# Optimization experiments

Measured on AMD Instinct MI355X. Metric: run time of the kernel, lower is better.

## Reference

```python
import jax, jax.numpy as jnp
import numpy as np

B, S, T = 64, 128, 64
V, E, H, L = 32000, 512, 512, 2
PAD, BOS = 0, 1


def setup_inputs() -> dict:
    key = jax.random.key(0)
    ks = jax.random.split(key, 14)
    w = lambda k, shape: (jax.random.normal(k, shape, jnp.float32) * 0.05)
    src_emb = w(ks[0], (V, E)).at[PAD].set(0.0)
    tgt_emb = w(ks[1], (V, E)).at[PAD].set(0.0)
    enc_Wih = w(ks[2], (L, 4 * H, E))
    enc_Whh = w(ks[3], (L, 4 * H, H))
    enc_b = w(ks[4], (L, 4 * H))          # b_ih + b_hh fused
    dec_Wih = w(ks[5], (L, 4 * H, E))
    dec_Whh = w(ks[6], (L, 4 * H, H))
    dec_b = w(ks[7], (L, 4 * H))
    gen_W = w(ks[8], (V, H))
    gen_b = jnp.zeros((V,), jnp.float32)
    x_seqs = jax.random.randint(ks[9], (B, S), 0, V, jnp.int32)
    x_len = jnp.sort(jax.random.randint(ks[10], (B,), 1, S + 1, jnp.int32))[::-1]
    y_seqs = jax.random.randint(ks[11], (B, T), 0, V, jnp.int32)
    teacher = jax.random.randint(ks[12], (T - 1,), 0, 2, jnp.int32)
    return dict(x_seqs=x_seqs, x_len=x_len, y_seqs=y_seqs, teacher=teacher,
                src_emb=src_emb, tgt_emb=tgt_emb,
                enc_Wih=enc_Wih, enc_Whh=enc_Whh, enc_b=enc_b,
                dec_Wih=dec_Wih, dec_Whh=dec_Whh, dec_b=dec_b,
                gen_W=gen_W, gen_b=gen_b)


def lstm_cell(x, h, c, Wih, Whh, b):
    # torch gate order: i, f, g, o
    g = x @ Wih.T + h @ Whh.T + b
    i, f, gg, o = jnp.split(g, 4, axis=-1)
    c2 = jax.nn.sigmoid(f) * c + jax.nn.sigmoid(i) * jnp.tanh(gg)
    h2 = jax.nn.sigmoid(o) * jnp.tanh(c2)
    return h2, c2


def encode(x_seqs, x_len, src_emb, Wih, Whh, b):
    emb = src_emb[x_seqs]                                  # [B,S,E]
    mask = jnp.arange(S)[None, :] < x_len[:, None]         # [B,S] valid steps
    inp = emb.transpose(1, 0, 2)                           # [S,B,E]
    m_t = mask.T                                           # [S,B]
    hs, cs = [], []
    for l in range(L):
        def step(carry, xs, l=l):
            h, c = carry
            xt, m = xs
            h2, c2 = lstm_cell(xt, h, c, Wih[l], Whh[l], b[l])
            m = m[:, None]
            h2 = jnp.where(m, h2, h)   # freeze state past sequence length
            c2 = jnp.where(m, c2, c)
            return (h2, c2), h2
        z = jnp.zeros((B, H), inp.dtype)
        (hT, cT), out = jax.lax.scan(step, (z, z), (inp, m_t))
        inp = out
        hs.append(hT)
        cs.append(cT)
    return jnp.stack(hs), jnp.stack(cs)                    # each [L,B,H]


def reference(x_seqs, x_len, y_seqs, teacher, src_emb, tgt_emb,
              enc_Wih, enc_Whh, enc_b, dec_Wih, dec_Whh, dec_b, gen_W, gen_b):
    h0, c0 = encode(x_seqs, x_len, src_emb, enc_Wih, enc_Whh, enc_b)

    def step(carry, xs):
        h, c, inp = carry                                  # [L,B,H],[L,B,H],[B]
        y_t, tf = xs                                       # [B], scalar flag
        x = tgt_emb[inp]                                   # [B,E]
        new_h, new_c = [], []
        for l in range(L):
            hl, cl = lstm_cell(x, h[l], c[l], dec_Wih[l], dec_Whh[l], dec_b[l])
            new_h.append(hl); new_c.append(cl)
            x = hl
        logp = jax.nn.log_softmax(x @ gen_W.T + gen_b, axis=-1)   # [B,V]
        expct = jnp.take_along_axis(logp, y_t[:, None], axis=1)[:, 0]
        pred = jnp.argmax(logp, axis=1).astype(inp.dtype)
        nxt = jnp.where(tf > 0, y_t, pred)                 # scheduled sampling
        return (jnp.stack(new_h), jnp.stack(new_c), nxt), expct

    inp0 = jnp.full((B,), BOS, jnp.int32)
    _, outp = jax.lax.scan(step, (h0, c0, inp0), (y_seqs[:, 1:].T, teacher))
    return outp.T                                          # [B, T-1]
```

## Files before the change

### kernel.cpp

```cpp
#include <hip/hip_runtime.h>
#include <hip/hip_bf16.h>
#include <cstdint>
#include <cstddef>

namespace {

constexpr int B = 64, S = 128, T = 64, V = 32000, E = 512, H = 512;
constexpr int G4 = 2048;
constexpr int TM1 = T - 1;
constexpr int CHUNK = 32;
constexpr int BH = B * H;
constexpr int NT = 128;
constexpr int NTILES = V / NT;
constexpr float MARGIN = 0.02f;
constexpr unsigned NBLK = 256;

typedef __attribute__((ext_vector_type(8))) short short8v;
typedef __attribute__((ext_vector_type(4))) float f32x4;

struct GemmSh { float As[16][68]; float Bs[16][132]; };
struct StepSh { float gs[64][17]; };
struct GenSh  { float lds[64][NT + 4]; float pv1[64][4], pv2[64][4], psum[64][4], mrow[64];
                int pi1[64][4], pi2[64][4]; };
struct RedSh  { float sM[256], sS[256], red[256]; float cV[16], rV[16]; int cI[16]; int cN, nxt; };

__device__ __forceinline__ float sigf(float x) { return 1.0f / (1.0f + expf(-x)); }

__device__ __forceinline__ void split3(float w, __hip_bfloat16& a, __hip_bfloat16& b,
                                       __hip_bfloat16& c2) {
    a = __float2bfloat16(w);
    float r = w - __bfloat162float(a);
    b = __float2bfloat16(r);
    c2 = __float2bfloat16(r - __bfloat162float(b));
}


__device__ __forceinline__ unsigned ld_coh_u32(const unsigned* p) {
    unsigned v;
    asm volatile("global_load_dword %0, %1, off sc0 sc1\n\ts_waitcnt vmcnt(0)"
                 : "=v"(v) : "v"(p) : "memory");
    return v;
}
__device__ __forceinline__ void st_coh_u32(unsigned* p, unsigned v) {
    asm volatile("global_store_dword %0, %1, off sc0 sc1" :: "v"(p), "v"(v) : "memory");
}
__device__ __forceinline__ float ld_coh_f32(const float* p) {
    float v;
    asm volatile("global_load_dword %0, %1, off sc0 sc1\n\ts_waitcnt vmcnt(0)"
                 : "=v"(v) : "v"(p));
    return v;
}
__device__ __forceinline__ void st_coh_f32(float* p, float v) {
    asm volatile("global_store_dword %0, %1, off sc0 sc1" :: "v"(p), "v"(v));
}
__device__ __forceinline__ f32x4 ld_coh_f32x4(const float* p) {
    f32x4 v;
    asm volatile("global_load_dwordx4 %0, %1, off sc0 sc1\n\ts_waitcnt vmcnt(0)"
                 : "=v"(v) : "v"(p));
    return v;
}
__device__ __forceinline__ void st_coh_b16(__hip_bfloat16* p, __hip_bfloat16 v) {
    unsigned short us; __builtin_memcpy(&us, &v, 2);
    unsigned u = us;
    asm volatile("global_store_short %0, %1, off sc0 sc1" :: "v"(p), "v"(u));
}
__device__ __forceinline__ void st_coh_b128(__hip_bfloat16* p, short8v v) {
    asm volatile("global_store_dwordx4 %0, %1, off sc0 sc1" :: "v"(p), "v"(v));
}
__device__ __forceinline__ void fence_vm() {
    asm volatile("s_waitcnt vmcnt(0)" ::: "memory");
}

__device__ __forceinline__ void ldg12(const __hip_bfloat16* p0, const __hip_bfloat16* p1,
                                      const __hip_bfloat16* p2, short8v* q)
{
    asm volatile(
        "global_load_dwordx4 %0, %12, off sc0 sc1\n\t"
        "global_load_dwordx4 %1, %12, off offset:64 sc0 sc1\n\t"
        "global_load_dwordx4 %2, %12, off offset:128 sc0 sc1\n\t"
        "global_load_dwordx4 %3, %12, off offset:192 sc0 sc1\n\t"
        "global_load_dwordx4 %4, %13, off sc0 sc1\n\t"
        "global_load_dwordx4 %5, %13, off offset:64 sc0 sc1\n\t"
        "global_load_dwordx4 %6, %13, off offset:128 sc0 sc1\n\t"
        "global_load_dwordx4 %7, %13, off offset:192 sc0 sc1\n\t"
        "global_load_dwordx4 %8, %14, off sc0 sc1\n\t"
        "global_load_dwordx4 %9, %14, off offset:64 sc0 sc1\n\t"
        "global_load_dwordx4 %10, %14, off offset:128 sc0 sc1\n\t"
        "global_load_dwordx4 %11, %14, off offset:192 sc0 sc1\n\t"
        "s_waitcnt vmcnt(0)"
        : "=&v"(q[0]), "=&v"(q[1]), "=&v"(q[2]), "=&v"(q[3]),
          "=&v"(q[4]), "=&v"(q[5]), "=&v"(q[6]), "=&v"(q[7]),
          "=&v"(q[8]), "=&v"(q[9]), "=&v"(q[10]), "=&v"(q[11])
        : "v"(p0), "v"(p1), "v"(p2));
}

__device__ __forceinline__ void ldg16(const __hip_bfloat16* p0, const __hip_bfloat16* p1,
                                      const __hip_bfloat16* p2, const __hip_bfloat16* p3,
                                      short8v* q)
{
    asm volatile(
        "global_load_dwordx4 %0, %16, off sc0 sc1\n\t"
        "global_load_dwordx4 %1, %16, off offset:64 sc0 sc1\n\t"
        "global_load_dwordx4 %2, %16, off offset:128 sc0 sc1\n\t"
        "global_load_dwordx4 %3, %16, off offset:192 sc0 sc1\n\t"
        "global_load_dwordx4 %4, %17, off sc0 sc1\n\t"
        "global_load_dwordx4 %5, %17, off offset:64 sc0 sc1\n\t"
        "global_load_dwordx4 %6, %17, off offset:128 sc0 sc1\n\t"
        "global_load_dwordx4 %7, %17, off offset:192 sc0 sc1\n\t"
        "global_load_dwordx4 %8, %18, off sc0 sc1\n\t"
        "global_load_dwordx4 %9, %18, off offset:64 sc0 sc1\n\t"
        "global_load_dwordx4 %10, %18, off offset:128 sc0 sc1\n\t"
        "global_load_dwordx4 %11, %18, off offset:192 sc0 sc1\n\t"
        "global_load_dwordx4 %12, %19, off sc0 sc1\n\t"
        "global_load_dwordx4 %13, %19, off offset:64 sc0 sc1\n\t"
        "global_load_dwordx4 %14, %19, off offset:128 sc0 sc1\n\t"
        "global_load_dwordx4 %15, %19, off offset:192 sc0 sc1\n\t"
        "s_waitcnt vmcnt(0)"
        : "=&v"(q[0]), "=&v"(q[1]), "=&v"(q[2]), "=&v"(q[3]),
          "=&v"(q[4]), "=&v"(q[5]), "=&v"(q[6]), "=&v"(q[7]),
          "=&v"(q[8]), "=&v"(q[9]), "=&v"(q[10]), "=&v"(q[11]),
          "=&v"(q[12]), "=&v"(q[13]), "=&v"(q[14]), "=&v"(q[15])
        : "v"(p0), "v"(p1), "v"(p2), "v"(p3));
}

__device__ __forceinline__ void ldg8(const __hip_bfloat16* p0, const __hip_bfloat16* p1,
                                     short8v* q)
{
    asm volatile(
        "global_load_dwordx4 %0, %8, off sc0 sc1\n\t"
        "global_load_dwordx4 %1, %8, off offset:64 sc0 sc1\n\t"
        "global_load_dwordx4 %2, %8, off offset:128 sc0 sc1\n\t"
        "global_load_dwordx4 %3, %8, off offset:192 sc0 sc1\n\t"
        "global_load_dwordx4 %4, %9, off sc0 sc1\n\t"
        "global_load_dwordx4 %5, %9, off offset:64 sc0 sc1\n\t"
        "global_load_dwordx4 %6, %9, off offset:128 sc0 sc1\n\t"
        "global_load_dwordx4 %7, %9, off offset:192 sc0 sc1\n\t"
        "s_waitcnt vmcnt(0)"
        : "=&v"(q[0]), "=&v"(q[1]), "=&v"(q[2]), "=&v"(q[3]),
          "=&v"(q[4]), "=&v"(q[5]), "=&v"(q[6]), "=&v"(q[7])
        : "v"(p0), "v"(p1));
}

__device__ __forceinline__ void gbar(unsigned* flags, unsigned* rel, unsigned& ep)
{
    unsigned tgt = ++ep;
    fence_vm();
    __syncthreads();
    const int tid = threadIdx.x;
    if (blockIdx.x == 0) {
        if (tid > 0) {
            int spins = 0;
            while (ld_coh_u32(&flags[tid * 32]) < tgt) {
                if (spins < 8) __builtin_amdgcn_s_sleep(1);
                else           __builtin_amdgcn_s_sleep(32);
                if (++spins > (1 << 16)) break;
            }
        }
        __syncthreads();
        st_coh_u32(&rel[tid * 32], tgt);
    } else {
        if (tid == 0) {
            st_coh_u32(&flags[blockIdx.x * 32], tgt);
            int spins = 0;
            while (ld_coh_u32(&rel[blockIdx.x * 32]) < tgt) {
                if (spins < 8) __builtin_amdgcn_s_sleep(1);
                else           __builtin_amdgcn_s_sleep(32);
                if (++spins > (1 << 16)) break;
            }
        }
        __syncthreads();
    }
}

__global__ __launch_bounds__(256)
void split_dec_k(const float* __restrict__ Wih, const float* __restrict__ Whh,
                 const float* __restrict__ bsrc,
                 __hip_bfloat16* __restrict__ P0, __hip_bfloat16* __restrict__ P1,
                 __hip_bfloat16* __restrict__ P2, float* __restrict__ bint)
{
    int row = blockIdx.x;
    int l = row >> 11, jp = row & 2047;
    int kh = jp >> 2, g = jp & 3, src = g * 512 + kh;
    const float* wih = Wih + ((size_t)l * 2048 + src) * 512;
    const float* whh = Whh + ((size_t)l * 2048 + src) * 512;
    size_t ro = (size_t)row * 1024;
    for (int k = threadIdx.x; k < 1024; k += 256) {
        float w = (k < 512) ? whh[k] : wih[k - 512];
        __hip_bfloat16 a, b, c2; split3(w, a, b, c2);
        P0[ro + k] = a; P1[ro + k] = b; P2[ro + k] = c2;
    }
    if (threadIdx.x == 0) bint[row] = bsrc[l * 2048 + src];
}

__global__ __launch_bounds__(256)
void split_enc_k(const float* __restrict__ Whh,
                 __hip_bfloat16* __restrict__ P0, __hip_bfloat16* __restrict__ P1,
                 __hip_bfloat16* __restrict__ P2)
{
    int row = blockIdx.x;
    int kh = row >> 2, g = row & 3, src = g * 512 + kh;
    const float* whh = Whh + (size_t)src * 512;
    size_t ro = (size_t)row * 512;
    for (int k = threadIdx.x; k < 512; k += 256) {
        __hip_bfloat16 a, b, c2; split3(whh[k], a, b, c2);
        P0[ro + k] = a; P1[ro + k] = b; P2[ro + k] = c2;
    }
}

__device__ void gemm_tile(char* shraw, const float* __restrict__ A,
                          const float* __restrict__ Wt, const float* __restrict__ bias,
                          float* __restrict__ C,
                          const int* __restrict__ xseq, int m0, int bx, int by)
{
    GemmSh* sh = reinterpret_cast<GemmSh*>(shraw);
    constexpr int K = 512, BK = 16;
    int tid = threadIdx.x;
    int bm = by * 64, bn = bx * 128;
    int tx = tid & 15, ty = tid >> 4;
    float acc[4][8] = {};

    int lm = tid >> 2, lk = (tid & 3) << 2;
    const float* Arow;
    {
        int mg = m0 + bm + lm; int tt = mg >> 6, b = mg & 63;
        Arow = A + (size_t)xseq[b * S + tt] * K;
    }
    int ln = tid >> 1, lkb = (tid & 1) << 3;
    const float* Brow = Wt + (size_t)(bn + ln) * K;

    for (int k0 = 0; k0 < K; k0 += BK) {
        float4 av = *(const float4*)(Arow + k0 + lk);
        sh->As[lk + 0][lm] = av.x; sh->As[lk + 1][lm] = av.y;
        sh->As[lk + 2][lm] = av.z; sh->As[lk + 3][lm] = av.w;
        float4 bv0 = *(const float4*)(Brow + k0 + lkb);
        float4 bv1 = *(const float4*)(Brow + k0 + lkb + 4);
        sh->Bs[lkb + 0][ln] = bv0.x; sh->Bs[lkb + 1][ln] = bv0.y;
        sh->Bs[lkb + 2][ln] = bv0.z; sh->Bs[lkb + 3][ln] = bv0.w;
        sh->Bs[lkb + 4][ln] = bv1.x; sh->Bs[lkb + 5][ln] = bv1.y;
        sh->Bs[lkb + 6][ln] = bv1.z; sh->Bs[lkb + 7][ln] = bv1.w;
        __syncthreads();
#pragma unroll
        for (int kk = 0; kk < BK; ++kk) {
            const float4 a4  = *(const float4*)&sh->As[kk][ty * 4];
            const float4 b4a = *(const float4*)&sh->Bs[kk][tx * 8];
            const float4 b4b = *(const float4*)&sh->Bs[kk][tx * 8 + 4];
            const float a[4]  = {a4.x, a4.y, a4.z, a4.w};
            const float bb[8] = {b4a.x, b4a.y, b4a.z, b4a.w,
                                 b4b.x, b4b.y, b4b.z, b4b.w};
#pragma unroll
            for (int i = 0; i < 4; ++i)
#pragma unroll
                for (int j = 0; j < 8; ++j)
                    acc[i][j] = fmaf(a[i], bb[j], acc[i][j]);
        }
        __syncthreads();
    }
#pragma unroll
    for (int i = 0; i < 4; ++i) {
        size_t crow = (size_t)(bm + ty * 4 + i) * G4;
#pragma unroll
        for (int j = 0; j < 8; ++j) {
            int cg = bn + tx * 8 + j;
            int jp = ((cg & 511) << 2) | (cg >> 9);
            st_coh_f32(C + crow + jp, acc[i][j] + bias[cg]);
        }
    }
}

template<int KHALF, bool ADDXC, bool MASK>
__device__ void step_body(char* shraw, int blk,
    const __hip_bfloat16* __restrict__ hA0, const __hip_bfloat16* __restrict__ hA1,
    const __hip_bfloat16* __restrict__ hA2,
    const __hip_bfloat16* __restrict__ xA0, const __hip_bfloat16* __restrict__ xA1,
    const __hip_bfloat16* __restrict__ xA2,
    const __hip_bfloat16* __restrict__ W0, const __hip_bfloat16* __restrict__ W1,
    const __hip_bfloat16* __restrict__ W2,
    const float* __restrict__ addsrc, const float* __restrict__ h_in,
    float* __restrict__ h_out, float* __restrict__ c,
    __hip_bfloat16* __restrict__ o0, __hip_bfloat16* __restrict__ o1,
    __hip_bfloat16* __restrict__ o2,
    const int* __restrict__ x_len, int t)
{
    StepSh* sh = reinterpret_cast<StepSh*>(shraw);
    int tid = threadIdx.x;
    int wave = tid >> 6, lane = tid & 63;
    int lr = lane & 15, kg = (lane >> 4) * 8;
    int arow = wave * 16 + lr;
    int brow = blk * 16 + lr;
    const int KW = 512 * KHALF;

    f32x4 acc0 = {0,0,0,0}, acc1 = {0,0,0,0}, acc2 = {0,0,0,0};
    const size_t aoff = (size_t)arow * 512 + kg;
    const size_t boff = (size_t)brow * KW + kg;

#pragma unroll
    for (int g = 0; g < KHALF * 4; ++g) {
        const __hip_bfloat16 *A0, *A1, *A2; size_t go;
        if (KHALF == 2 && g >= 4) { A0 = xA0; A1 = xA1; A2 = xA2;
                                    go = aoff + (size_t)(g - 4) * 128; }
        else                      { A0 = hA0; A1 = hA1; A2 = hA2;
                                    go = aoff + (size_t)g * 128; }
        short8v q[12];
        ldg12(A0 + go, A1 + go, A2 + go, q);
#pragma unroll
        for (int j = 0; j < 4; ++j) {
            int k0 = g * 128 + j * 32;
            short8v b0 = *(const short8v*)(W0 + boff + k0);
            short8v b1 = *(const short8v*)(W1 + boff + k0);
            short8v b2 = *(const short8v*)(W2 + boff + k0);
            short8v a0 = q[j], a1 = q[4 + j], a2 = q[8 + j];
            acc0 = __builtin_amdgcn_mfma_f32_16x16x32_bf16(a0, b0, acc0, 0, 0, 0);
            acc1 = __builtin_amdgcn_mfma_f32_16x16x32_bf16(a0, b1, acc1, 0, 0, 0);
            acc2 = __builtin_amdgcn_mfma_f32_16x16x32_bf16(a1, b0, acc2, 0, 0, 0);
            acc0 = __builtin_amdgcn_mfma_f32_16x16x32_bf16(a1, b1, acc0, 0, 0, 0);
            acc1 = __builtin_amdgcn_mfma_f32_16x16x32_bf16(a0, b2, acc1, 0, 0, 0);
            acc2 = __builtin_amdgcn_mfma_f32_16x16x32_bf16(a2, b0, acc2, 0, 0, 0);
        }
    }
    int rb = (lane >> 4) * 4;
#pragma unroll
    for (int r = 0; r < 4; ++r)
        sh->gs[wave * 16 + rb + r][lr] = acc0[r] + acc1[r] + acc2[r];
    __syncthreads();

    int b = tid >> 2, khl = tid & 3;
    int khg = blk * 4 + khl;
    f32x4 add;
    if (ADDXC) add = ld_coh_f32x4(addsrc + (size_t)b * G4 + (size_t)khg * 4);
    else       add = *(const f32x4*)(addsrc + (size_t)khg * 4);
    float gi = sh->gs[b][khl * 4 + 0] + add[0];
    float gf = sh->gs[b][khl * 4 + 1] + add[1];
    float gg = sh->gs[b][khl * 4 + 2] + add[2];
    float go2 = sh->gs[b][khl * 4 + 3] + add[3];
    size_t idx = (size_t)b * H + khg;
    float cold = ld_coh_f32(c + idx);
    float c2 = sigf(gf) * cold + sigf(gi) * tanhf(gg);
    float h2 = sigf(go2) * tanhf(c2);
    if (MASK) {
        bool mk = t < x_len[b];
        if (!mk) { h2 = ld_coh_f32(h_in + idx); c2 = cold; }
    }
    if (h_out) st_coh_f32(h_out + idx, h2);
    st_coh_f32(c + idx, c2);
    __hip_bfloat16 s0, s1, s2; split3(h2, s0, s1, s2);
    st_coh_b16(o0 + idx, s0); st_coh_b16(o1 + idx, s1); st_coh_b16(o2 + idx, s2);
}

__device__ void gen_body(char* shraw, int bid,
                         const __hip_bfloat16* __restrict__ hbf,
                         const __hip_bfloat16* __restrict__ Wbf,
                         const float* __restrict__ genb,
                         float* __restrict__ part)
{
    GenSh* sh = reinterpret_cast<GenSh*>(shraw);
    int tid = threadIdx.x;
    int wave = tid >> 6, lane = tid & 63;
    int n0 = bid * NT;
    int lr = lane & 15;
    int kg = (lane >> 4) * 8;

    f32x4 acc[4][2];
    const f32x4 zero = {0.f, 0.f, 0.f, 0.f};
#pragma unroll
    for (int i = 0; i < 4; ++i)
#pragma unroll
        for (int j = 0; j < 2; ++j) acc[i][j] = zero;

    const __hip_bfloat16* Arow = hbf + (size_t)lr * 512 + kg;
    const __hip_bfloat16* Brow = Wbf + (size_t)(n0 + wave * 32 + lr) * 512 + kg;
#pragma unroll
    for (int g = 0; g < 4; ++g) {
        short8v qa[16], qb[8];
        ldg16(Arow + g * 128, Arow + 8192 + g * 128,
              Arow + 16384 + g * 128, Arow + 24576 + g * 128, qa);
        ldg8(Brow + g * 128, Brow + 8192 + g * 128, qb);
#pragma unroll
        for (int j = 0; j < 4; ++j) {
#pragma unroll
            for (int mf = 0; mf < 4; ++mf)
#pragma unroll
                for (int nf = 0; nf < 2; ++nf)
                    acc[mf][nf] = __builtin_amdgcn_mfma_f32_16x16x32_bf16(
                        qa[mf * 4 + j], qb[nf * 4 + j], acc[mf][nf], 0, 0, 0);
        }
    }
#pragma unroll
    for (int nf = 0; nf < 2; ++nf) {
        int colLocal = wave * 32 + nf * 16 + lr;
        float bias = genb[n0 + colLocal];
#pragma unroll
        for (int mf = 0; mf < 4; ++mf) {
#pragma unroll
            for (int r = 0; r < 4; ++r) {
                int row = mf * 16 + (lane >> 4) * 4 + r;
                sh->lds[row][colLocal] = acc[mf][nf][r] + bias;
            }
        }
    }
    __syncthreads();

    int row = tid >> 2, q = tid & 3;
    int cbase = q * 32;
    float v1 = -3.4e38f, v2 = -3.4e38f; int i1 = 0x7fffffff, i2 = 0x7fffffff;
    for (int c = 0; c < 32; ++c) {
        float v = sh->lds[row][cbase + c];
        int ci = cbase + c;
        if (v > v1 || (v == v1 && ci < i1)) { v2 = v1; i2 = i1; v1 = v; i1 = ci; }
        else if (v > v2 || (v == v2 && ci < i2)) { v2 = v; i2 = ci; }
    }
    sh->pv1[row][q] = v1; sh->pi1[row][q] = i1; sh->pv2[row][q] = v2; sh->pi2[row][q] = i2;
    __syncthreads();

    float t1 = -3.4e38f, t2 = -3.4e38f; int j1 = 0x7fffffff, j2 = 0x7fffffff;
    if (q == 0) {
        for (int k = 0; k < 4; ++k) {
            float a1 = sh->pv1[row][k]; int a1i = sh->pi1[row][k];
            float a2 = sh->pv2[row][k]; int a2i = sh->pi2[row][k];
            if (a1 > t1 || (a1 == t1 && a1i < j1)) { t2 = t1; j2 = j1; t1 = a1; j1 = a1i; }
            else if (a1 > t2 || (a1 == t2 && a1i < j2)) { t2 = a1; j2 = a1i; }
            if (a2 > t1 || (a2 == t1 && a2i < j1)) { t2 = t1; j2 = j1; t1 = a2; j1 = a2i; }
            else if (a2 > t2 || (a2 == t2 && a2i < j2)) { t2 = a2; j2 = a2i; }
        }
        sh->mrow[row] = t1;
    }
    __syncthreads();
    float m = sh->mrow[row];
    float s = 0.f;
    for (int c = 0; c < 32; ++c) s += expf(sh->lds[row][cbase + c] - m);
    sh->psum[row][q] = s;
    __syncthreads();
    if (q == 0) {
        float sum = sh->psum[row][0] + sh->psum[row][1] + sh->psum[row][2] + sh->psum[row][3];
        float* p = part + ((size_t)bid * B + row) * 6;
        st_coh_f32(p + 0, t1);
        st_coh_f32(p + 1, t2);
        st_coh_u32((unsigned*)(p + 2), (unsigned)(n0 + j1));
        st_coh_u32((unsigned*)(p + 3), (unsigned)(n0 + j2));
        st_coh_f32(p + 4, sum);
    }
}

__device__ void reduce_body(char* shraw, int b,
                            const float* __restrict__ part,
                            const float* __restrict__ h,
                            const float* __restrict__ genW, const float* __restrict__ genb,
                            const float* __restrict__ tgt_emb,
                            const int* __restrict__ y_seqs, const int* __restrict__ teacher,
                            float* __restrict__ outp,
                            __hip_bfloat16* __restrict__ xp0, __hip_bfloat16* __restrict__ xp1,
                            __hip_bfloat16* __restrict__ xp2, int t)
{
    RedSh* sh = reinterpret_cast<RedSh*>(shraw);
    int tid = threadIdx.x;
    int y = y_seqs[b * T + t + 1];
    const float* hrow = h + (size_t)b * 512;
    float h_a = ld_coh_f32(hrow + tid);
    float h_b = ld_coh_f32(hrow + tid + 256);

    float p_top1 = -3.4e38f, p_top2 = -3.4e38f, p_sum = 0.f;
    int p_i1 = 0x7fffffff, p_i2 = 0x7fffffff;
    if (tid < NTILES) {
        const float* p = part + ((size_t)tid * B + b) * 6;
        f32x4 v4 = ld_coh_f32x4(p);
        p_top1 = v4[0]; p_top2 = v4[1];
        p_i1 = __float_as_int(v4[2]);
        p_i2 = __float_as_int(v4[3]);
        p_sum = ld_coh_f32(p + 4);
    }
    sh->sM[tid] = p_top1; __syncthreads();
    for (int o = 128; o; o >>= 1) { if (tid < o) sh->sM[tid] = fmaxf(sh->sM[tid], sh->sM[tid + o]); __syncthreads(); }
    float M = sh->sM[0];
    if (tid == 0) sh->cN = 0;
    __syncthreads();

    float Ssum = (tid < NTILES) ? p_sum * expf(p_top1 - M) : 0.f;
    if (tid < NTILES) {
        if (p_top1 >= M - MARGIN) { int j = atomicAdd(&sh->cN, 1); if (j < 16) { sh->cV[j] = p_top1; sh->cI[j] = p_i1; } }
        if (p_top2 >= M - MARGIN) { int j = atomicAdd(&sh->cN, 1); if (j < 16) { sh->cV[j] = p_top2; sh->cI[j] = p_i2; } }
    }
    sh->sS[tid] = Ssum; __syncthreads();
    for (int o = 128; o; o >>= 1) { if (tid < o) sh->sS[tid] += sh->sS[tid + o]; __syncthreads(); }
    float lse = M + logf(sh->sS[0]);
    int nc = sh->cN < 16 ? sh->cN : 16;

    {
        const float* wrow = genW + (size_t)y * 512;
        float s = fmaf(h_a, wrow[tid], 0.f) + h_b * wrow[tid + 256];
        sh->red[tid] = s; __syncthreads();
        for (int o = 128; o; o >>= 1) { if (tid < o) sh->red[tid] += sh->red[tid + o]; __syncthreads(); }
        if (tid == 0) outp[b * TM1 + t] = sh->red[0] + genb[y] - lse;
        __syncthreads();
    }
    if (nc > 1) {
        for (int j = 0; j < nc; ++j) {
            const float* wrow = genW + (size_t)sh->cI[j] * 512;
            float s = fmaf(h_a, wrow[tid], 0.f) + h_b * wrow[tid + 256];
            sh->red[tid] = s; __syncthreads();
            for (int o = 128; o; o >>= 1) { if (tid < o) sh->red[tid] += sh->red[tid + o]; __syncthreads(); }
            if (tid == 0) sh->rV[j] = sh->red[0] + genb[sh->cI[j]];
            __syncthreads();
        }
    }
    if (tid == 0) {
        int winner;
        if (nc == 1) winner = sh->cI[0];
        else {
            float bv = -3.4e38f; int bi = 0x7fffffff;
            for (int j = 0; j < nc; ++j)
                if (sh->rV[j] > bv || (sh->rV[j] == bv && sh->cI[j] < bi)) { bv = sh->rV[j]; bi = sh->cI[j]; }
            winner = bi;
        }
        sh->nxt = (teacher[t] > 0) ? y : winner;
    }
    __syncthreads();
    int tok = sh->nxt;
    for (int k = tid; k < 512; k += 256) {
        float w = tgt_emb[(size_t)tok * 512 + k];
        __hip_bfloat16 s0, s1, s2; split3(w, s0, s1, s2);
        st_coh_b16(xp0 + (size_t)b * 512 + k, s0);
        st_coh_b16(xp1 + (size_t)b * 512 + k, s1);
        st_coh_b16(xp2 + (size_t)b * 512 + k, s2);
    }
}

struct Args {
    const int *x_seqs, *x_len, *y_seqs, *teacher;
    const float *src_emb, *tgt_emb, *eWih, *eb, *genW, *genb;
    float* Xc;
    const __hip_bfloat16 *eP0, *eP1, *eP2;
    const __hip_bfloat16 *e1P0, *e1P1, *e1P2;
    const float* ebint;
    const __hip_bfloat16 *dP0, *dP1, *dP2;
    const float* bint;
    float *hf32, *cbuf, *dech1;
    __hip_bfloat16 *P, *xP, *Wbf;
    float* part;
    float* outp;
    unsigned *flags, *rel;
};

__global__ __launch_bounds__(256, 1)
void persist_k(Args a)
{
    __shared__ __align__(16) char shpool[40960];
    unsigned ep = 0;
    const int bid = blockIdx.x;
    const int tid = threadIdx.x;
    const int gtid = bid * 256 + tid;
    const int GS = NBLK * 256;

    auto Pl = [&](int l, int slot, int pl) {
        return a.P + (((size_t)(l * 2 + slot)) * 3 + pl) * BH; };

    for (int i = gtid; i < BH; i += GS) {
        st_coh_f32(a.hf32 + i, 0.f); st_coh_f32(a.hf32 + 2 * BH + i, 0.f);
        st_coh_f32(a.cbuf + i, 0.f); st_coh_f32(a.cbuf + BH + i, 0.f);
    }
    {
        unsigned* p0 = (unsigned*)Pl(0, 0, 0);
        unsigned* p1 = (unsigned*)Pl(1, 0, 0);
        for (int i = gtid; i < 3 * BH / 2; i += GS) { st_coh_u32(p0 + i, 0u); st_coh_u32(p1 + i, 0u); }
    }
    gbar(a.flags, a.rel, ep);

    for (int c0 = 0; c0 < S; c0 += CHUNK) {
        for (int tile = bid; tile < 512; tile += NBLK)
            gemm_tile(shpool, a.src_emb, a.eWih, a.eb, a.Xc,
                      a.x_seqs, c0 * B, tile & 15, tile >> 4);
        gbar(a.flags, a.rel, ep);
        for (int tl = 0; tl < CHUNK; ++tl) {
            int t = c0 + tl;
            if (bid < 128) {
                step_body<1, true, true>(shpool, bid,
                    Pl(0, t & 1, 0), Pl(0, t & 1, 1), Pl(0, t & 1, 2),
                    nullptr, nullptr, nullptr,
                    a.eP0, a.eP1, a.eP2,
                    a.Xc + (size_t)tl * B * G4,
                    a.hf32 + (size_t)(t & 1) * BH, a.hf32 + (size_t)((t + 1) & 1) * BH,
                    a.cbuf,
                    Pl(0, (t + 1) & 1, 0), Pl(0, (t + 1) & 1, 1), Pl(0, (t + 1) & 1, 2),
                    a.x_len, t);
            } else if (t >= 1) {
                int u = t - 1;
                step_body<2, false, true>(shpool, bid - 128,
                    Pl(1, u & 1, 0), Pl(1, u & 1, 1), Pl(1, u & 1, 2),
                    Pl(0, t & 1, 0), Pl(0, t & 1, 1), Pl(0, t & 1, 2),
                    a.e1P0, a.e1P1, a.e1P2,
                    a.ebint,
                    a.hf32 + (size_t)(2 + (u & 1)) * BH, a.hf32 + (size_t)(2 + ((u + 1) & 1)) * BH,
                    a.cbuf + BH,
                    Pl(1, (u + 1) & 1, 0), Pl(1, (u + 1) & 1, 1), Pl(1, (u + 1) & 1, 2),
                    a.x_len, u);
            }
            gbar(a.flags, a.rel, ep);
        }
    }
    if (bid < 128) {
        int u = S - 1;
        step_body<2, false, true>(shpool, bid,
            Pl(1, u & 1, 0), Pl(1, u & 1, 1), Pl(1, u & 1, 2),
            Pl(0, (u + 1) & 1, 0), Pl(0, (u + 1) & 1, 1), Pl(0, (u + 1) & 1, 2),
            a.e1P0, a.e1P1, a.e1P2,
            a.ebint,
            a.hf32 + (size_t)(2 + (u & 1)) * BH, a.hf32 + (size_t)(2 + ((u + 1) & 1)) * BH,
            a.cbuf + BH,
            Pl(1, (u + 1) & 1, 0), Pl(1, (u + 1) & 1, 1), Pl(1, (u + 1) & 1, 2),
            a.x_len, u);
    }
    gbar(a.flags, a.rel, ep);

    {
        const int N8 = V * E / 8;
        for (int i = gtid; i < N8; i += GS) {
            float4 x = *(const float4*)(a.genW + (size_t)i * 8);
            float4 y = *(const float4*)(a.genW + (size_t)i * 8 + 4);
            __hip_bfloat16 tmp[8];
            tmp[0] = __float2bfloat16(x.x); tmp[1] = __float2bfloat16(x.y);
            tmp[2] = __float2bfloat16(x.z); tmp[3] = __float2bfloat16(x.w);
            tmp[4] = __float2bfloat16(y.x); tmp[5] = __float2bfloat16(y.y);
            tmp[6] = __float2bfloat16(y.z); tmp[7] = __float2bfloat16(y.w);
            st_coh_b128(a.Wbf + (size_t)i * 8, *(const short8v*)tmp);
        }
        for (int i = gtid; i < BH; i += GS) {
            int k = i & 511;
            float w = a.tgt_emb[512 + k];
            __hip_bfloat16 s0, s1, s2; split3(w, s0, s1, s2);
            st_coh_b16(a.xP + i, s0);
            st_coh_b16(a.xP + BH + i, s1);
            st_coh_b16(a.xP + 2 * BH + i, s2);
        }
    }
    gbar(a.flags, a.rel, ep);

    for (int t = 0; t < TM1; ++t) {
        int si = t & 1, so = si ^ 1;
        if (bid < 128)
            step_body<2, false, false>(shpool, bid,
                Pl(0, si, 0), Pl(0, si, 1), Pl(0, si, 2),
                a.xP, a.xP + BH, a.xP + 2 * BH,
                a.dP0, a.dP1, a.dP2, a.bint,
                nullptr, nullptr, a.cbuf,
                Pl(0, so, 0), Pl(0, so, 1), Pl(0, so, 2),
                nullptr, 0);
        gbar(a.flags, a.rel, ep);
        if (bid < 128)
            step_body<2, false, false>(shpool, bid,
                Pl(1, si, 0), Pl(1, si, 1), Pl(1, si, 2),
                Pl(0, so, 0), Pl(0, so, 1), Pl(0, so, 2),
                a.dP0 + (size_t)G4 * 1024, a.dP1 + (size_t)G4 * 1024,
                a.dP2 + (size_t)G4 * 1024, a.bint + G4,
                nullptr, a.dech1, a.cbuf + BH,
                Pl(1, so, 0), Pl(1, so, 1), Pl(1, so, 2),
                nullptr, 0);
        gbar(a.flags, a.rel, ep);
        if (bid < NTILES)
            gen_body(shpool, bid, Pl(1, so, 0), a.Wbf, a.genb, a.part);
        gbar(a.flags, a.rel, ep);
        if (bid < B)
            reduce_body(shpool, bid, a.part, a.dech1, a.genW, a.genb, a.tgt_emb,
                        a.y_seqs, a.teacher, a.outp,
                        a.xP, a.xP + BH, a.xP + 2 * BH, t);
        gbar(a.flags, a.rel, ep);
    }
}

}

extern "C" void kernel_launch(void* const* d_in, const int* in_sizes, int n_in,
                              void* d_out, int out_size, void* d_ws, size_t ws_size,
                              hipStream_t stream)
{
    (void)in_sizes; (void)n_in; (void)out_size;
    const int*   x_seqs  = (const int*)  d_in[0];
    const int*   x_len   = (const int*)  d_in[1];
    const int*   y_seqs  = (const int*)  d_in[2];
    const int*   teacher = (const int*)  d_in[3];
    const float* src_emb = (const float*)d_in[4];
    const float* tgt_emb = (const float*)d_in[5];
    const float* eWih    = (const float*)d_in[6];
    const float* eWhh    = (const float*)d_in[7];
    const float* eb      = (const float*)d_in[8];
    const float* dWih    = (const float*)d_in[9];
    const float* dWhh    = (const float*)d_in[10];
    const float* db      = (const float*)d_in[11];
    const float* genW    = (const float*)d_in[12];
    const float* genb    = (const float*)d_in[13];

    float* w = (float*)d_ws;
    size_t off = 0;
    auto take = [&](size_t n) { float* p = w + off; off += n; return p; };
    auto takeb = [&](size_t n) { return (__hip_bfloat16*)take((n + 1) / 2); };

    unsigned* flags = (unsigned*)take(256 * 32);
    unsigned* rel   = (unsigned*)take(256 * 32);
    float* Xc = take((size_t)CHUNK * B * G4);
    __hip_bfloat16* eP0  = takeb((size_t)G4 * 512);
    __hip_bfloat16* eP1  = takeb((size_t)G4 * 512);
    __hip_bfloat16* eP2  = takeb((size_t)G4 * 512);
    __hip_bfloat16* e1P0 = takeb((size_t)G4 * 1024);
    __hip_bfloat16* e1P1 = takeb((size_t)G4 * 1024);
    __hip_bfloat16* e1P2 = takeb((size_t)G4 * 1024);
    float* ebint = take((size_t)G4);
    __hip_bfloat16* dP0 = takeb((size_t)2 * G4 * 1024);
    __hip_bfloat16* dP1 = takeb((size_t)2 * G4 * 1024);
    __hip_bfloat16* dP2 = takeb((size_t)2 * G4 * 1024);
    float* bint  = take(2 * (size_t)G4);
    float* hf32  = take(4 * (size_t)BH);
    float* cbuf  = take(2 * (size_t)BH);
    float* dech1 = take((size_t)BH);
    __hip_bfloat16* P  = takeb((size_t)12 * BH);
    __hip_bfloat16* xP = takeb((size_t)3 * BH);
    float* part_f = take((size_t)NTILES * B * 6);
    if (ws_size < off * sizeof(float)) return;

    dim3 tpb256(256);
    split_enc_k<<<dim3(G4), tpb256, 0, stream>>>(eWhh, eP0, eP1, eP2);
    split_dec_k<<<dim3(G4), tpb256, 0, stream>>>(
        eWih + (size_t)G4 * E, eWhh + (size_t)G4 * E, eb + G4, e1P0, e1P1, e1P2, ebint);
    split_dec_k<<<dim3(2 * G4), tpb256, 0, stream>>>(
        dWih, dWhh, db, dP0, dP1, dP2, bint);
    hipError_t _e = hipMemsetAsync(flags, 0, 2 * 256 * 32 * sizeof(unsigned), stream);
    (void)_e;

    Args a;
    a.x_seqs = x_seqs; a.x_len = x_len; a.y_seqs = y_seqs; a.teacher = teacher;
    a.src_emb = src_emb; a.tgt_emb = tgt_emb; a.eWih = eWih; a.eb = eb;
    a.genW = genW; a.genb = genb;
    a.Xc = Xc;
    a.eP0 = eP0; a.eP1 = eP1; a.eP2 = eP2;
    a.e1P0 = e1P0; a.e1P1 = e1P1; a.e1P2 = e1P2; a.ebint = ebint;
    a.dP0 = dP0; a.dP1 = dP1; a.dP2 = dP2; a.bint = bint;
    a.hf32 = hf32; a.cbuf = cbuf; a.dech1 = dech1;
    a.P = P; a.xP = xP;
    a.Wbf = (__hip_bfloat16*)Xc;
    a.part = part_f;
    a.outp = (float*)d_out;
    a.flags = flags; a.rel = rel;

    persist_k<<<dim3(NBLK), tpb256, 0, stream>>>(a);
}
```

Baseline: 10.36 ms.

## Widen LSTM step tiles to 64 columns and version decoder state buffers per step

Each step block now computes 64 gate columns instead of 16, so the recurrent steps run on 32 blocks instead of 128, with vectorized state stores. Decoder hidden, input and embedding planes become per-timestep versioned buffers, which lets the step and reduce kernels read them through normal cached loads instead of coherent loads. The generator now reads A fragments directly instead of bulk coherent loads, and the barrier spin uses a fixed sleep. The aim is to cut coherent-load traffic and per-step sync cost, at the price of fewer active blocks and more workspace memory.

New measurement: 22.24 ms. 2.15x slower.

```diff
diff --git a/kernel.cpp b/kernel.cpp
--- a/kernel.cpp
+++ b/kernel.cpp
@@ -17,9 +17,10 @@
 
 typedef __attribute__((ext_vector_type(8))) short short8v;
 typedef __attribute__((ext_vector_type(4))) float f32x4;
+typedef __attribute__((ext_vector_type(2))) unsigned u32x2;
 
 struct GemmSh { float As[16][68]; float Bs[16][132]; };
-struct StepSh { float gs[64][17]; };
+struct StepSh { float gs[64][68]; };
 struct GenSh  { float lds[64][NT + 4]; float pv1[64][4], pv2[64][4], psum[64][4], mrow[64];
                 int pi1[64][4], pi2[64][4]; };
 struct RedSh  { float sM[256], sS[256], red[256]; float cV[16], rV[16]; int cI[16]; int cN, nxt; };
@@ -33,7 +34,9 @@
     b = __float2bfloat16(r);
     c2 = __float2bfloat16(r - __bfloat162float(b));
 }
-
+__device__ __forceinline__ unsigned short bf16bits(__hip_bfloat16 v) {
+    unsigned short u; __builtin_memcpy(&u, &v, 2); return u;
+}
 
 __device__ __forceinline__ unsigned ld_coh_u32(const unsigned* p) {
     unsigned v;
@@ -59,10 +62,11 @@
                  : "=v"(v) : "v"(p));
     return v;
 }
-__device__ __forceinline__ void st_coh_b16(__hip_bfloat16* p, __hip_bfloat16 v) {
-    unsigned short us; __builtin_memcpy(&us, &v, 2);
-    unsigned u = us;
-    asm volatile("global_store_short %0, %1, off sc0 sc1" :: "v"(p), "v"(u));
+__device__ __forceinline__ void st_coh_f32x4(float* p, f32x4 v) {
+    asm volatile("global_store_dwordx4 %0, %1, off sc0 sc1" :: "v"(p), "v"(v));
+}
+__device__ __forceinline__ void st_coh_b64(__hip_bfloat16* p, u32x2 v) {
+    asm volatile("global_store_dwordx2 %0, %1, off sc0 sc1" :: "v"(p), "v"(v));
 }
 __device__ __forceinline__ void st_coh_b128(__hip_bfloat16* p, short8v v) {
     asm volatile("global_store_dwordx4 %0, %1, off sc0 sc1" :: "v"(p), "v"(v));
@@ -94,35 +98,6 @@
         : "v"(p0), "v"(p1), "v"(p2));
 }
 
-__device__ __forceinline__ void ldg16(const __hip_bfloat16* p0, const __hip_bfloat16* p1,
-                                      const __hip_bfloat16* p2, const __hip_bfloat16* p3,
-                                      short8v* q)
-{
-    asm volatile(
-        "global_load_dwordx4 %0, %16, off sc0 sc1\n\t"
-        "global_load_dwordx4 %1, %16, off offset:64 sc0 sc1\n\t"
-        "global_load_dwordx4 %2, %16, off offset:128 sc0 sc1\n\t"
-        "global_load_dwordx4 %3, %16, off offset:192 sc0 sc1\n\t"
-        "global_load_dwordx4 %4, %17, off sc0 sc1\n\t"
-        "global_load_dwordx4 %5, %17, off offset:64 sc0 sc1\n\t"
-        "global_load_dwordx4 %6, %17, off offset:128 sc0 sc1\n\t"
-        "global_load_dwordx4 %7, %17, off offset:192 sc0 sc1\n\t"
-        "global_load_dwordx4 %8, %18, off sc0 sc1\n\t"
-        "global_load_dwordx4 %9, %18, off offset:64 sc0 sc1\n\t"
-        "global_load_dwordx4 %10, %18, off offset:128 sc0 sc1\n\t"
-        "global_load_dwordx4 %11, %18, off offset:192 sc0 sc1\n\t"
-        "global_load_dwordx4 %12, %19, off sc0 sc1\n\t"
-        "global_load_dwordx4 %13, %19, off offset:64 sc0 sc1\n\t"
-        "global_load_dwordx4 %14, %19, off offset:128 sc0 sc1\n\t"
-        "global_load_dwordx4 %15, %19, off offset:192 sc0 sc1\n\t"
-        "s_waitcnt vmcnt(0)"
-        : "=&v"(q[0]), "=&v"(q[1]), "=&v"(q[2]), "=&v"(q[3]),
-          "=&v"(q[4]), "=&v"(q[5]), "=&v"(q[6]), "=&v"(q[7]),
-          "=&v"(q[8]), "=&v"(q[9]), "=&v"(q[10]), "=&v"(q[11]),
-          "=&v"(q[12]), "=&v"(q[13]), "=&v"(q[14]), "=&v"(q[15])
-        : "v"(p0), "v"(p1), "v"(p2), "v"(p3));
-}
-
 __device__ __forceinline__ void ldg8(const __hip_bfloat16* p0, const __hip_bfloat16* p1,
                                      short8v* q)
 {
@@ -151,9 +126,8 @@
         if (tid > 0) {
             int spins = 0;
             while (ld_coh_u32(&flags[tid * 32]) < tgt) {
-                if (spins < 8) __builtin_amdgcn_s_sleep(1);
-                else           __builtin_amdgcn_s_sleep(32);
-                if (++spins > (1 << 16)) break;
+                __builtin_amdgcn_s_sleep(4);
+                if (++spins > (1 << 17)) break;
             }
         }
         __syncthreads();
@@ -163,9 +137,8 @@
             st_coh_u32(&flags[blockIdx.x * 32], tgt);
             int spins = 0;
             while (ld_coh_u32(&rel[blockIdx.x * 32]) < tgt) {
-                if (spins < 8) __builtin_amdgcn_s_sleep(1);
-                else           __builtin_amdgcn_s_sleep(32);
-                if (++spins > (1 << 16)) break;
+                __builtin_amdgcn_s_sleep(4);
+                if (++spins > (1 << 17)) break;
             }
         }
         __syncthreads();
@@ -267,7 +240,7 @@
     }
 }
 
-template<int KHALF, bool ADDXC, bool MASK>
+template<int KHALF, bool ADDXC, bool MASK, bool CACHED>
 __device__ void step_body(char* shraw, int blk,
     const __hip_bfloat16* __restrict__ hA0, const __hip_bfloat16* __restrict__ hA1,
     const __hip_bfloat16* __restrict__ hA2,
@@ -286,12 +259,19 @@
     int wave = tid >> 6, lane = tid & 63;
     int lr = lane & 15, kg = (lane >> 4) * 8;
     int arow = wave * 16 + lr;
-    int brow = blk * 16 + lr;
     const int KW = 512 * KHALF;
-
-    f32x4 acc0 = {0,0,0,0}, acc1 = {0,0,0,0}, acc2 = {0,0,0,0};
     const size_t aoff = (size_t)arow * 512 + kg;
-    const size_t boff = (size_t)brow * KW + kg;
+    size_t boff[4];
+#pragma unroll
+    for (int ct = 0; ct < 4; ++ct)
+        boff[ct] = (size_t)(blk * 64 + ct * 16 + lr) * KW + kg;
+
+    f32x4 acc[4][3];
+    const f32x4 zero = {0.f, 0.f, 0.f, 0.f};
+#pragma unroll
+    for (int ct = 0; ct < 4; ++ct)
+#pragma unroll
+        for (int p = 0; p < 3; ++p) acc[ct][p] = zero;
 
 #pragma unroll
     for (int g = 0; g < KHALF * 4; ++g) {
@@ -300,50 +280,85 @@
                                     go = aoff + (size_t)(g - 4) * 128; }
         else                      { A0 = hA0; A1 = hA1; A2 = hA2;
                                     go = aoff + (size_t)g * 128; }
-        short8v q[12];
-        ldg12(A0 + go, A1 + go, A2 + go, q);
+        short8v qa[12];
+        if (CACHED) {
+#pragma unroll
+            for (int j = 0; j < 4; ++j) {
+                qa[j]     = *(const short8v*)(A0 + go + j * 32);
+                qa[4 + j] = *(const short8v*)(A1 + go + j * 32);
+                qa[8 + j] = *(const short8v*)(A2 + go + j * 32);
+            }
+        } else {
+            ldg12(A0 + go, A1 + go, A2 + go, qa);
+        }
 #pragma unroll
         for (int j = 0; j < 4; ++j) {
             int k0 = g * 128 + j * 32;
-            short8v b0 = *(const short8v*)(W0 + boff + k0);
-            short8v b1 = *(const short8v*)(W1 + boff + k0);
-            short8v b2 = *(const short8v*)(W2 + boff + k0);
-            short8v a0 = q[j], a1 = q[4 + j], a2 = q[8 + j];
-            acc0 = __builtin_amdgcn_mfma_f32_16x16x32_bf16(a0, b0, acc0, 0, 0, 0);
-            acc1 = __builtin_amdgcn_mfma_f32_16x16x32_bf16(a0, b1, acc1, 0, 0, 0);
-            acc2 = __builtin_amdgcn_mfma_f32_16x16x32_bf16(a1, b0, acc2, 0, 0, 0);
-            acc0 = __builtin_amdgcn_mfma_f32_16x16x32_bf16(a1, b1, acc0, 0, 0, 0);
-            acc1 = __builtin_amdgcn_mfma_f32_16x16x32_bf16(a0, b2, acc1, 0, 0, 0);
-            acc2 = __builtin_amdgcn_mfma_f32_16x16x32_bf16(a2, b0, acc2, 0, 0, 0);
+            short8v a0 = qa[j], a1 = qa[4 + j], a2 = qa[8 + j];
+#pragma unroll
+            for (int ct = 0; ct < 4; ++ct) {
+                short8v b0 = *(const short8v*)(W0 + boff[ct] + k0);
+                short8v b1 = *(const short8v*)(W1 + boff[ct] + k0);
+                short8v b2 = *(const short8v*)(W2 + boff[ct] + k0);
+                acc[ct][0] = __builtin_amdgcn_mfma_f32_16x16x32_bf16(a0, b0, acc[ct][0], 0, 0, 0);
+                acc[ct][1] = __builtin_amdgcn_mfma_f32_16x16x32_bf16(a0, b1, acc[ct][1], 0, 0, 0);
+                acc[ct][2] = __builtin_amdgcn_mfma_f32_16x16x32_bf16(a1, b0, acc[ct][2], 0, 0, 0);
+                acc[ct][0] = __builtin_amdgcn_mfma_f32_16x16x32_bf16(a1, b1, acc[ct][0], 0, 0, 0);
+                acc[ct][1] = __builtin_amdgcn_mfma_f32_16x16x32_bf16(a0, b2, acc[ct][1], 0, 0, 0);
+                acc[ct][2] = __builtin_amdgcn_mfma_f32_16x16x32_bf16(a2, b0, acc[ct][2], 0, 0, 0);
+            }
         }
     }
     int rb = (lane >> 4) * 4;
 #pragma unroll
     for (int r = 0; r < 4; ++r)
-        sh->gs[wave * 16 + rb + r][lr] = acc0[r] + acc1[r] + acc2[r];
+#pragma unroll
+        for (int ct = 0; ct < 4; ++ct)
+            sh->gs[wave * 16 + rb + r][ct * 16 + lr] =
+                acc[ct][0][r] + acc[ct][1][r] + acc[ct][2][r];
     __syncthreads();
 
-    int b = tid >> 2, khl = tid & 3;
-    int khg = blk * 4 + khl;
-    f32x4 add;
-    if (ADDXC) add = ld_coh_f32x4(addsrc + (size_t)b * G4 + (size_t)khg * 4);
-    else       add = *(const f32x4*)(addsrc + (size_t)khg * 4);
-    float gi = sh->gs[b][khl * 4 + 0] + add[0];
-    float gf = sh->gs[b][khl * 4 + 1] + add[1];
-    float gg = sh->gs[b][khl * 4 + 2] + add[2];
-    float go2 = sh->gs[b][khl * 4 + 3] + add[3];
-    size_t idx = (size_t)b * H + khg;
-    float cold = ld_coh_f32(c + idx);
-    float c2 = sigf(gf) * cold + sigf(gi) * tanhf(gg);
-    float h2 = sigf(go2) * tanhf(c2);
-    if (MASK) {
-        bool mk = t < x_len[b];
-        if (!mk) { h2 = ld_coh_f32(h_in + idx); c2 = cold; }
-    }
-    if (h_out) st_coh_f32(h_out + idx, h2);
-    st_coh_f32(c + idx, c2);
-    __hip_bfloat16 s0, s1, s2; split3(h2, s0, s1, s2);
-    st_coh_b16(o0 + idx, s0); st_coh_b16(o1 + idx, s1); st_coh_b16(o2 + idx, s2);
+    int b = tid >> 2, q = tid & 3;
+    int m0 = q * 4;
+    int khg0 = blk * 16 + m0;
+    size_t idx0 = (size_t)b * H + khg0;
+    f32x4 cold4 = ld_coh_f32x4(c + idx0);
+    f32x4 hin4 = {0.f, 0.f, 0.f, 0.f};
+    bool mk = true;
+    if (MASK) { mk = (t < x_len[b]); if (!mk) hin4 = ld_coh_f32x4(h_in + idx0); }
+    f32x4 h4, c4;
+#pragma unroll
+    for (int kk = 0; kk < 4; ++kk) {
+        int m = m0 + kk;
+        f32x4 add;
+        if (ADDXC) add = ld_coh_f32x4(addsrc + (size_t)b * G4 + (size_t)(khg0 + kk) * 4);
+        else       add = *(const f32x4*)(addsrc + (size_t)(khg0 + kk) * 4);
+        float gi  = sh->gs[b][m * 4 + 0] + add[0];
+        float gf  = sh->gs[b][m * 4 + 1] + add[1];
+        float gg  = sh->gs[b][m * 4 + 2] + add[2];
+        float go2 = sh->gs[b][m * 4 + 3] + add[3];
+        float c2 = sigf(gf) * cold4[kk] + sigf(gi) * tanhf(gg);
+        float h2 = sigf(go2) * tanhf(c2);
+        if (MASK && !mk) { h2 = hin4[kk]; c2 = cold4[kk]; }
+        h4[kk] = h2; c4[kk] = c2;
+    }
+    st_coh_f32x4(c + idx0, c4);
+    if (h_out) st_coh_f32x4(h_out + idx0, h4);
+    unsigned short s0b[4], s1b[4], s2b[4];
+#pragma unroll
+    for (int kk = 0; kk < 4; ++kk) {
+        __hip_bfloat16 s0, s1, s2; split3(h4[kk], s0, s1, s2);
+        s0b[kk] = bf16bits(s0); s1b[kk] = bf16bits(s1); s2b[kk] = bf16bits(s2);
+    }
+    u32x2 p0 = {(unsigned)s0b[0] | ((unsigned)s0b[1] << 16),
+                (unsigned)s0b[2] | ((unsigned)s0b[3] << 16)};
+    u32x2 p1 = {(unsigned)s1b[0] | ((unsigned)s1b[1] << 16),
+                (unsigned)s1b[2] | ((unsigned)s1b[3] << 16)};
+    u32x2 p2 = {(unsigned)s2b[0] | ((unsigned)s2b[1] << 16),
+                (unsigned)s2b[2] | ((unsigned)s2b[3] << 16)};
+    st_coh_b64(o0 + idx0, p0);
+    st_coh_b64(o1 + idx0, p1);
+    st_coh_b64(o2 + idx0, p2);
 }
 
 __device__ void gen_body(char* shraw, int bid,
@@ -370,18 +385,18 @@
     const __hip_bfloat16* Brow = Wbf + (size_t)(n0 + wave * 32 + lr) * 512 + kg;
 #pragma unroll
     for (int g = 0; g < 4; ++g) {
-        short8v qa[16], qb[8];
-        ldg16(Arow + g * 128, Arow + 8192 + g * 128,
-              Arow + 16384 + g * 128, Arow + 24576 + g * 128, qa);
+        short8v qb[8];
         ldg8(Brow + g * 128, Brow + 8192 + g * 128, qb);
 #pragma unroll
         for (int j = 0; j < 4; ++j) {
 #pragma unroll
-            for (int mf = 0; mf < 4; ++mf)
+            for (int mf = 0; mf < 4; ++mf) {
+                short8v a = *(const short8v*)(Arow + (size_t)mf * 8192 + g * 128 + j * 32);
 #pragma unroll
                 for (int nf = 0; nf < 2; ++nf)
                     acc[mf][nf] = __builtin_amdgcn_mfma_f32_16x16x32_bf16(
-                        qa[mf * 4 + j], qb[nf * 4 + j], acc[mf][nf], 0, 0, 0);
+                        a, qb[nf * 4 + j], acc[mf][nf], 0, 0, 0);
+            }
         }
     }
 #pragma unroll
@@ -454,8 +469,8 @@
     int tid = threadIdx.x;
     int y = y_seqs[b * T + t + 1];
     const float* hrow = h + (size_t)b * 512;
-    float h_a = ld_coh_f32(hrow + tid);
-    float h_b = ld_coh_f32(hrow + tid + 256);
+    float h_a = hrow[tid];
+    float h_b = hrow[tid + 256];
 
     float p_top1 = -3.4e38f, p_top2 = -3.4e38f, p_sum = 0.f;
     int p_i1 = 0x7fffffff, p_i2 = 0x7fffffff;
@@ -517,9 +532,12 @@
     for (int k = tid; k < 512; k += 256) {
         float w = tgt_emb[(size_t)tok * 512 + k];
         __hip_bfloat16 s0, s1, s2; split3(w, s0, s1, s2);
-        st_coh_b16(xp0 + (size_t)b * 512 + k, s0);
-        st_coh_b16(xp1 + (size_t)b * 512 + k, s1);
-        st_coh_b16(xp2 + (size_t)b * 512 + k, s2);
+        st_coh_b16_helper: ;
+        unsigned short u0 = bf16bits(s0), u1 = bf16bits(s1), u2 = bf16bits(s2);
+        unsigned v0 = u0, v1 = u1, v2 = u2;
+        asm volatile("global_store_short %0, %1, off sc0 sc1" :: "v"(xp0 + (size_t)b * 512 + k), "v"(v0));
+        asm volatile("global_store_short %0, %1, off sc0 sc1" :: "v"(xp1 + (size_t)b * 512 + k), "v"(v1));
+        asm volatile("global_store_short %0, %1, off sc0 sc1" :: "v"(xp2 + (size_t)b * 512 + k), "v"(v2));
     }
 }
 
@@ -532,8 +550,10 @@
     const float* ebint;
     const __hip_bfloat16 *dP0, *dP1, *dP2;
     const float* bint;
-    float *hf32, *cbuf, *dech1;
-    __hip_bfloat16 *P, *xP, *Wbf;
+    float *hf32, *cbuf;
+    __hip_bfloat16 *P, *Wbf;
+    __hip_bfloat16 *L0v, *L1v, *Xv;
+    float* dh1v;
     float* part;
     float* outp;
     unsigned *flags, *rel;
@@ -549,8 +569,11 @@
     const int gtid = bid * 256 + tid;
     const int GS = NBLK * 256;
 
-    auto Pl = [&](int l, int slot, int pl) {
+    auto Pl  = [&](int l, int slot, int pl) {
         return a.P + (((size_t)(l * 2 + slot)) * 3 + pl) * BH; };
+    auto L0v = [&](int slot, int pl) { return a.L0v + ((size_t)slot * 3 + pl) * BH; };
+    auto L1v = [&](int slot, int pl) { return a.L1v + ((size_t)slot * 3 + pl) * BH; };
+    auto Xv  = [&](int slot, int pl) { return a.Xv  + ((size_t)slot * 3 + pl) * BH; };
 
     for (int i = gtid; i < BH; i += GS) {
         st_coh_f32(a.hf32 + i, 0.f); st_coh_f32(a.hf32 + 2 * BH + i, 0.f);
@@ -570,8 +593,8 @@
         gbar(a.flags, a.rel, ep);
         for (int tl = 0; tl < CHUNK; ++tl) {
             int t = c0 + tl;
-            if (bid < 128) {
-                step_body<1, true, true>(shpool, bid,
+            if (bid < 32) {
+                step_body<1, true, true, false>(shpool, bid,
                     Pl(0, t & 1, 0), Pl(0, t & 1, 1), Pl(0, t & 1, 2),
                     nullptr, nullptr, nullptr,
                     a.eP0, a.eP1, a.eP2,
@@ -580,9 +603,9 @@
                     a.cbuf,
                     Pl(0, (t + 1) & 1, 0), Pl(0, (t + 1) & 1, 1), Pl(0, (t + 1) & 1, 2),
                     a.x_len, t);
-            } else if (t >= 1) {
+            } else if (bid < 64 && t >= 1) {
                 int u = t - 1;
-                step_body<2, false, true>(shpool, bid - 128,
+                step_body<2, false, true, false>(shpool, bid - 32,
                     Pl(1, u & 1, 0), Pl(1, u & 1, 1), Pl(1, u & 1, 2),
                     Pl(0, t & 1, 0), Pl(0, t & 1, 1), Pl(0, t & 1, 2),
                     a.e1P0, a.e1P1, a.e1P2,
@@ -595,9 +618,9 @@
             gbar(a.flags, a.rel, ep);
         }
     }
-    if (bid < 128) {
+    if (bid < 32) {
         int u = S - 1;
-        step_body<2, false, true>(shpool, bid,
+        step_body<2, false, true, false>(shpool, bid,
             Pl(1, u & 1, 0), Pl(1, u & 1, 1), Pl(1, u & 1, 2),
             Pl(0, (u + 1) & 1, 0), Pl(0, (u + 1) & 1, 1), Pl(0, (u + 1) & 1, 2),
             a.e1P0, a.e1P1, a.e1P2,
@@ -621,45 +644,54 @@
             tmp[6] = __float2bfloat16(y.z); tmp[7] = __float2bfloat16(y.w);
             st_coh_b128(a.Wbf + (size_t)i * 8, *(const short8v*)tmp);
         }
+        const unsigned* s0 = (const unsigned*)Pl(0, 0, 0);
+        const unsigned* s1 = (const unsigned*)Pl(1, 0, 0);
+        unsigned* d0 = (unsigned*)L0v(0, 0);
+        unsigned* d1 = (unsigned*)L1v(0, 0);
+        for (int i = gtid; i < 3 * BH / 2; i += GS) {
+            st_coh_u32(d0 + i, ld_coh_u32(s0 + i));
+            st_coh_u32(d1 + i, ld_coh_u32(s1 + i));
+        }
         for (int i = gtid; i < BH; i += GS) {
             int k = i & 511;
             float w = a.tgt_emb[512 + k];
-            __hip_bfloat16 s0, s1, s2; split3(w, s0, s1, s2);
-            st_coh_b16(a.xP + i, s0);
-            st_coh_b16(a.xP + BH + i, s1);
-            st_coh_b16(a.xP + 2 * BH + i, s2);
+            __hip_bfloat16 s0v, s1v, s2v; split3(w, s0v, s1v, s2v);
+            unsigned v0 = bf16bits(s0v), v1 = bf16bits(s1v), v2 = bf16bits(s2v);
+            asm volatile("global_store_short %0, %1, off sc0 sc1" :: "v"(Xv(0,0) + i), "v"(v0));
+            asm volatile("global_store_short %0, %1, off sc0 sc1" :: "v"(Xv(0,1) + i), "v"(v1));
+            asm volatile("global_store_short %0, %1, off sc0 sc1" :: "v"(Xv(0,2) + i), "v"(v2));
         }
     }
     gbar(a.flags, a.rel, ep);
 
     for (int t = 0; t < TM1; ++t) {
-        int si = t & 1, so = si ^ 1;
-        if (bid < 128)
-            step_body<2, false, false>(shpool, bid,
-                Pl(0, si, 0), Pl(0, si, 1), Pl(0, si, 2),
-                a.xP, a.xP + BH, a.xP + 2 * BH,
+        if (bid < 32)
+            step_body<2, false, false, true>(shpool, bid,
+                L0v(t, 0), L0v(t, 1), L0v(t, 2),
+                Xv(t, 0), Xv(t, 1), Xv(t, 2),
                 a.dP0, a.dP1, a.dP2, a.bint,
                 nullptr, nullptr, a.cbuf,
-                Pl(0, so, 0), Pl(0, so, 1), Pl(0, so, 2),
+                L0v(t + 1, 0), L0v(t + 1, 1), L0v(t + 1, 2),
                 nullptr, 0);
         gbar(a.flags, a.rel, ep);
-        if (bid < 128)
-            step_body<2, false, false>(shpool, bid,
-                Pl(1, si, 0), Pl(1, si, 1), Pl(1, si, 2),
-                Pl(0, so, 0), Pl(0, so, 1), Pl(0, so, 2),
+        if (bid < 32)
+            step_body<2, false, false, true>(shpool, bid,
+                L1v(t, 0), L1v(t, 1), L1v(t, 2),
+                L0v(t + 1, 0), L0v(t + 1, 1), L0v(t + 1, 2),
                 a.dP0 + (size_t)G4 * 1024, a.dP1 + (size_t)G4 * 1024,
                 a.dP2 + (size_t)G4 * 1024, a.bint + G4,
-                nullptr, a.dech1, a.cbuf + BH,
-                Pl(1, so, 0), Pl(1, so, 1), Pl(1, so, 2),
+                nullptr, a.dh1v + (size_t)(t + 1) * BH, a.cbuf + BH,
+                L1v(t + 1, 0), L1v(t + 1, 1), L1v(t + 1, 2),
                 nullptr, 0);
         gbar(a.flags, a.rel, ep);
         if (bid < NTILES)
-            gen_body(shpool, bid, Pl(1, so, 0), a.Wbf, a.genb, a.part);
+            gen_body(shpool, bid, L1v(t + 1, 0), a.Wbf, a.genb, a.part);
         gbar(a.flags, a.rel, ep);
         if (bid < B)
-            reduce_body(shpool, bid, a.part, a.dech1, a.genW, a.genb, a.tgt_emb,
+            reduce_body(shpool, bid, a.part, a.dh1v + (size_t)(t + 1) * BH,
+                        a.genW, a.genb, a.tgt_emb,
                         a.y_seqs, a.teacher, a.outp,
-                        a.xP, a.xP + BH, a.xP + 2 * BH, t);
+                        Xv(t + 1, 0), Xv(t + 1, 1), Xv(t + 1, 2), t);
         gbar(a.flags, a.rel, ep);
     }
 }
@@ -707,9 +739,11 @@
     float* bint  = take(2 * (size_t)G4);
     float* hf32  = take(4 * (size_t)BH);
     float* cbuf  = take(2 * (size_t)BH);
-    float* dech1 = take((size_t)BH);
     __hip_bfloat16* P  = takeb((size_t)12 * BH);
-    __hip_bfloat16* xP = takeb((size_t)3 * BH);
+    __hip_bfloat16* L0v = takeb((size_t)(TM1 + 1) * 3 * BH);
+    __hip_bfloat16* L1v = takeb((size_t)(TM1 + 1) * 3 * BH);
+    __hip_bfloat16* Xv  = takeb((size_t)(TM1 + 1) * 3 * BH);
+    float* dh1v = take((size_t)(TM1 + 1) * BH);
     float* part_f = take((size_t)NTILES * B * 6);
     if (ws_size < off * sizeof(float)) return;
 
@@ -730,9 +764,9 @@
     a.eP0 = eP0; a.eP1 = eP1; a.eP2 = eP2;
     a.e1P0 = e1P0; a.e1P1 = e1P1; a.e1P2 = e1P2; a.ebint = ebint;
     a.dP0 = dP0; a.dP1 = dP1; a.dP2 = dP2; a.bint = bint;
-    a.hf32 = hf32; a.cbuf = cbuf; a.dech1 = dech1;
-    a.P = P; a.xP = xP;
-    a.Wbf = (__hip_bfloat16*)Xc;
+    a.hf32 = hf32; a.cbuf = cbuf;
+    a.P = P; a.Wbf = (__hip_bfloat16*)Xc;
+    a.L0v = L0v; a.L1v = L1v; a.Xv = Xv; a.dh1v = dh1v;
     a.part = part_f;
     a.outp = (float*)d_out;
     a.flags = flags; a.rel = rel;
```
